# Kernel tuning notes

Measured on AMD Instinct MI355X. Metric: run time of the kernel, lower is better.

The kernel has to match this reference:

```python
import jax, jax.numpy as jnp
import numpy as np

D, H, L, DFF, V = 512, 8, 6, 2048, 32000
PAD = 0

def make_pe(max_len, d):
    pos = jnp.arange(max_len, dtype=jnp.float32)[:, None]
    div = jnp.exp(jnp.arange(0, d, 2, dtype=jnp.float32) * (-np.log(10000.0) / d))
    ang = pos * div  # [max_len, d/2]
    pe = jnp.zeros((max_len, d), jnp.float32)
    pe = pe.at[:, 0::2].set(jnp.sin(ang)).at[:, 1::2].set(jnp.cos(ang))
    return pe

def layernorm(x, g, b, eps=1e-5):
    m = x.mean(-1, keepdims=True)
    v = ((x - m) ** 2).mean(-1, keepdims=True)
    return (x - m) * jax.lax.rsqrt(v + eps) * g + b

def mha(q_in, k_in, v_in, W, Bv, mask):
    # W: [4, D, D] (q,k,v,out); Bv: [4, D]; mask broadcastable to [B,H,Tq,Tk] bool
    b, sq, d = q_in.shape
    hd = d // H
    def proj(x, w, bb):
        y = x @ w + bb
        return y.reshape(x.shape[0], x.shape[1], H, hd).transpose(0, 2, 1, 3)  # bhsd
    Q, K, Vh = proj(q_in, W[0], Bv[0]), proj(k_in, W[1], Bv[1]), proj(v_in, W[2], Bv[2])
    scores = jnp.einsum('bhqd,bhkd->bhqk', Q, K) / np.sqrt(hd).astype(np.float32)
    scores = jnp.where(mask, scores, jnp.float32(-1e9))
    attn = jax.nn.softmax(scores, axis=-1)
    ctx = jnp.einsum('bhqk,bhkd->bhqd', attn, Vh).transpose(0, 2, 1, 3).reshape(b, sq, d)
    return ctx @ W[3] + Bv[3]

def ffn(x, w1, b1, w2, b2):
    return jax.nn.relu(x @ w1 + b1) @ w2 + b2

def setup_inputs() -> dict:
    key = jax.random.key(0)
    ks = jax.random.split(key, 16)
    s = 0.02
    inp = {
        'src': jax.random.randint(ks[0], (8, 512), 0, V, dtype=jnp.int32),
        'tgt': jax.random.randint(ks[1], (8, 512), 0, V, dtype=jnp.int32),
        'src_emb': (jax.random.normal(ks[2], (V, D)) * s).at[PAD].set(0.0),
        'tgt_emb': (jax.random.normal(ks[3], (V, D)) * s).at[PAD].set(0.0),
        'enc_attn_w': jax.random.normal(ks[4], (L, 4, D, D)) * s,
        'enc_attn_b': jnp.zeros((L, 4, D)),
        'enc_ffn_w1': jax.random.normal(ks[5], (L, D, DFF)) * s,
        'enc_ffn_b1': jnp.zeros((L, DFF)),
        'enc_ffn_w2': jax.random.normal(ks[6], (L, DFF, D)) * s,
        'enc_ffn_b2': jnp.zeros((L, D)),
        'enc_ln_g': jnp.ones((L, 2, D)),
        'enc_ln_b': jnp.zeros((L, 2, D)),
        'dec_self_w': jax.random.normal(ks[7], (L, 4, D, D)) * s,
        'dec_self_b': jnp.zeros((L, 4, D)),
        'dec_cross_w': jax.random.normal(ks[8], (L, 4, D, D)) * s,
        'dec_cross_b': jnp.zeros((L, 4, D)),
        'dec_ffn_w1': jax.random.normal(ks[9], (L, D, DFF)) * s,
        'dec_ffn_b1': jnp.zeros((L, DFF)),
        'dec_ffn_w2': jax.random.normal(ks[10], (L, DFF, D)) * s,
        'dec_ffn_b2': jnp.zeros((L, D)),
        'dec_ln_g': jnp.ones((L, 3, D)),
        'dec_ln_b': jnp.zeros((L, 3, D)),
        'out_w': jax.random.normal(ks[11], (D, V)) * s,
        'out_b': jnp.zeros((V,)),
    }
    return inp

def reference(src, tgt, src_emb, tgt_emb, enc_attn_w, enc_attn_b, enc_ffn_w1, enc_ffn_b1,
              enc_ffn_w2, enc_ffn_b2, enc_ln_g, enc_ln_b, dec_self_w, dec_self_b,
              dec_cross_w, dec_cross_b, dec_ffn_w1, dec_ffn_b1, dec_ffn_w2, dec_ffn_b2,
              dec_ln_g, dec_ln_b, out_w, out_b):
    B_, S = src.shape
    T = tgt.shape[1]
    pe = make_pe(max(S, T), D)
    scale = jnp.float32(np.sqrt(D))

    src_pad = (src != PAD)[:, None, None, :]                    # [B,1,1,S]
    causal = jnp.tril(jnp.ones((T, T), bool))                   # [T,T]
    tgt_mask = (tgt != PAD)[:, None, None, :] & causal[None, None]  # [B,1,T,T]

    # encoder (dropout = identity at inference)
    x = src_emb[src] * scale + pe[None, :S]
    for i in range(L):
        a = mha(x, x, x, enc_attn_w[i], enc_attn_b[i], src_pad)
        x = layernorm(x + a, enc_ln_g[i, 0], enc_ln_b[i, 0])
        f = ffn(x, enc_ffn_w1[i], enc_ffn_b1[i], enc_ffn_w2[i], enc_ffn_b2[i])
        x = layernorm(x + f, enc_ln_g[i, 1], enc_ln_b[i, 1])
    memory = x

    # decoder
    y = tgt_emb[tgt] * scale + pe[None, :T]
    for i in range(L):
        a = mha(y, y, y, dec_self_w[i], dec_self_b[i], tgt_mask)
        y = layernorm(y + a, dec_ln_g[i, 0], dec_ln_b[i, 0])
        c = mha(y, memory, memory, dec_cross_w[i], dec_cross_b[i], src_pad)
        y = layernorm(y + c, dec_ln_g[i, 1], dec_ln_b[i, 1])
        f = ffn(y, dec_ffn_w1[i], dec_ffn_b1[i], dec_ffn_w2[i], dec_ffn_b2[i])
        y = layernorm(y + f, dec_ln_g[i, 2], dec_ln_b[i, 2])

    return y @ out_w + out_b  # [B, T, tgt_vocab]
```

## Files before the change

### kernel.cpp

```cpp
#include <hip/hip_runtime.h>
#include <hip/hip_bf16.h>


#define Dm 512
#define Hh 8
#define HD 64
#define Ll 6
#define DFFv 2048
#define Vv 32000
#define Bb 8
#define Ss 512
#define NTOK (Bb * Ss)

typedef __bf16 bf16x8 __attribute__((ext_vector_type(8)));
typedef __bf16 bf16x4 __attribute__((ext_vector_type(4)));
typedef float  f32x4  __attribute__((ext_vector_type(4)));

#define GLOAD16(gp, lp) __builtin_amdgcn_global_load_lds( \
    (const __attribute__((address_space(1))) unsigned int*)(const void*)(gp), \
    (__attribute__((address_space(3))) unsigned int*)(void*)(lp), 16, 0, 0)

__global__ void embed_pe_k(const int* __restrict__ tok, const float* __restrict__ emb,
                           float* __restrict__ out, __bf16* __restrict__ outb, int Slen)
{
    int row = blockIdx.x;
    int s = row % Slen;
    int t = tok[row];
    const float* e = emb + (size_t)t * Dm;
    float* o = out + (size_t)row * Dm;
    __bf16* ob = outb + (size_t)row * Dm;
    for (int dd = threadIdx.x; dd < Dm; dd += blockDim.x) {
        int j = dd >> 1;
        float div = expf((float)(2 * j) * (-9.210340371976184f / 512.0f));
        float ang = (float)s * div;
        float pe = (dd & 1) ? cosf(ang) : sinf(ang);
        float v = e[dd] * 22.627416997969522f + pe;
        o[dd] = v;
        ob[dd] = (__bf16)v;
    }
}

__global__ __launch_bounds__(256) void wtr_k(const float* __restrict__ W,
                                             __bf16* __restrict__ Wt, int K, int N)
{
    __shared__ float t[32][33];
    size_t msz = (size_t)K * N;
    const float* Wm = W + (size_t)blockIdx.z * msz;
    __bf16* Wtm = Wt + (size_t)blockIdx.z * msz;
    int n0 = blockIdx.x * 32, k0 = blockIdx.y * 32;
    int r = threadIdx.x >> 3, c4 = (threadIdx.x & 7) * 4;
    float4 v = *reinterpret_cast<const float4*>(&Wm[(size_t)(k0 + r) * N + n0 + c4]);
    t[r][c4] = v.x; t[r][c4 + 1] = v.y; t[r][c4 + 2] = v.z; t[r][c4 + 3] = v.w;
    __syncthreads();
    int n = threadIdx.x >> 3, kq = (threadIdx.x & 7) * 4;
    bf16x4 o;
    o[0] = (__bf16)t[kq + 0][n]; o[1] = (__bf16)t[kq + 1][n];
    o[2] = (__bf16)t[kq + 2][n]; o[3] = (__bf16)t[kq + 3][n];
    *reinterpret_cast<bf16x4*>(&Wtm[(size_t)(n0 + n) * K + k0 + kq]) = o;
}

template<int BM, int BN, int RELU, int MODE, int SWAPG>
__global__ __launch_bounds__(256) void gemm_mfma_k(const __bf16* __restrict__ A,
                                                   const __bf16* __restrict__ Wt,
                                                   const float* __restrict__ bias,
                                                   void* __restrict__ Cout,
                                                   __bf16* __restrict__ out_k,
                                                   __bf16* __restrict__ out_vT,
                                                   int M, int N, int K)
{
    constexpr int NF_M = BM / 32;
    constexpr int NF_N = BN / 32;
    __shared__ __bf16 As[2][BM * 32];
    __shared__ __bf16 Bs[2][BN * 32];
    const int tid = threadIdx.x;
    const int wave = tid >> 6, lane = tid & 63;
    const int wr = wave >> 1, wc = wave & 1;
    const int row0 = (SWAPG ? blockIdx.x : blockIdx.y) * BM;
    const int col0 = (SWAPG ? blockIdx.y : blockIdx.x) * BN;

    f32x4 acc[NF_M][NF_N] = {};

    const int rsub = lane >> 2;
    const int kel  = (lane & 3) * 8;
    const int fr   = lane & 15;
    const int kg   = lane >> 4;

    auto stage = [&](int buf, int k0) {
        #pragma unroll
        for (int cc = 0; cc < BM / 64; ++cc) {
            int c = wave * (BM / 64) + cc;
            GLOAD16(A + (size_t)(row0 + c * 16 + rsub) * K + k0 + kel,
                    &As[buf][c * 512 + lane * 8]);
        }
        #pragma unroll
        for (int cc = 0; cc < BN / 64; ++cc) {
            int c = wave * (BN / 64) + cc;
            GLOAD16(Wt + (size_t)(col0 + c * 16 + rsub) * K + k0 + kel,
                    &Bs[buf][c * 512 + lane * 8]);
        }
    };

    stage(0, 0);
    __syncthreads();

    const int nk = K >> 5;
    for (int kb = 0; kb < nk; ++kb) {
        int cur = kb & 1;
        if (kb + 1 < nk) stage(cur ^ 1, (kb + 1) * 32);

        const bf16x8* Av = reinterpret_cast<const bf16x8*>(As[cur]);
        const bf16x8* Bv = reinterpret_cast<const bf16x8*>(Bs[cur]);
        bf16x8 af[NF_M], bq[NF_N];
        #pragma unroll
        for (int m = 0; m < NF_M; ++m)
            af[m] = Av[(wr * (BM / 2) + m * 16 + fr) * 4 + kg];
        #pragma unroll
        for (int n = 0; n < NF_N; ++n)
            bq[n] = Bv[(wc * (BN / 2) + n * 16 + fr) * 4 + kg];
        #pragma unroll
        for (int m = 0; m < NF_M; ++m)
            #pragma unroll
            for (int n = 0; n < NF_N; ++n)
                acc[m][n] = __builtin_amdgcn_mfma_f32_16x16x32_bf16(
                    af[m], bq[n], acc[m][n], 0, 0, 0);
        __syncthreads();
    }

    #pragma unroll
    for (int m = 0; m < NF_M; ++m) {
        #pragma unroll
        for (int n = 0; n < NF_N; ++n) {
            int colg = col0 + wc * (BN / 2) + n * 16 + fr;
            float bv = bias[colg];
            #pragma unroll
            for (int j = 0; j < 4; ++j) {
                int row = row0 + wr * (BM / 2) + m * 16 + kg * 4 + j;
                float v = acc[m][n][j] + bv;
                if (RELU) v = fmaxf(v, 0.f);
                if constexpr (MODE == 0) {
                    ((float*)Cout)[(size_t)row * N + colg] = v;
                } else if constexpr (MODE == 1) {
                    ((__bf16*)Cout)[(size_t)row * N + colg] = (__bf16)v;
                } else {
                    int seg = colg >> 9;
                    int c = colg & 511;
                    bool isV = (MODE == 2) ? (seg == 2) : (seg == 1);
                    if (!isV) {
                        __bf16* o = (MODE == 2 && seg == 1) ? out_k : (__bf16*)Cout;
                        o[(size_t)row * 512 + c] = (__bf16)v;
                    } else {
                        int bi = row >> 9, s = row & 511;
                        int hh = c >> 6, f = c & 63;
                        out_vT[(size_t)((bi * 8 + hh) * 64 + f) * 512 + s] = (__bf16)v;
                    }
                }
            }
        }
    }
}

__global__ __launch_bounds__(256) void attn_mfma_k(const __bf16* __restrict__ Qb,
                                                   const __bf16* __restrict__ Kb,
                                                   const __bf16* __restrict__ VbT,
                                                   __bf16* __restrict__ Ob,
                                                   const int* __restrict__ key_tok,
                                                   int causal)
{
    __shared__ __bf16 Ks[2][128 * 64];
    __shared__ __bf16 Vs[2][64 * 128];
    __shared__ __bf16 Pl[4][16 * 128];

    const int tid = threadIdx.x;
    const int w = tid >> 6, lane = tid & 63;
    const int fr = lane & 15, kg = lane >> 4;
    const int q0 = blockIdx.x * 64;
    const int h = blockIdx.y, b = blockIdx.z;
    const int qrow = q0 + w * 16 + fr;
    const int swz = (fr & 7) << 4;

    bf16x8 qf[2];
    {
        const __bf16* qp = Qb + ((size_t)(b * 512 + qrow) * 512 + h * 64 + kg * 8);
        qf[0] = *reinterpret_cast<const bf16x8*>(qp);
        qf[1] = *reinterpret_cast<const bf16x8*>(qp + 32);
    }

    f32x4 po[4] = {};
    float m_run = -3.0e38f, l_run = 0.f;
    __bf16* pw = Pl[w];

    auto stage = [&](int buf, int kk0) {
        #pragma unroll
        for (int c = 0; c < 4; ++c) {
            int ch = c * 256 + tid;
            int r = ch >> 3, gsk = (ch & 7) ^ (r & 7);
            GLOAD16(Kb + ((size_t)(b * 512 + kk0 + r) * 512 + h * 64 + gsk * 8),
                    &Ks[buf][ch * 8]);
            int f = ch >> 4, gsv = (ch & 15) ^ (f & 7);
            GLOAD16(VbT + ((size_t)((b * 8 + h) * 64 + f) * 512 + kk0 + gsv * 8),
                    &Vs[buf][ch * 8]);
        }
    };

    const int kkend = causal ? ((q0 + 64 + 127) & ~127) : 512;
    stage(0, 0);
    __syncthreads();

    for (int kk0 = 0; kk0 < kkend; kk0 += 128) {
        int cur = (kk0 >> 7) & 1;
        if (kk0 + 128 < kkend) stage(cur ^ 1, kk0 + 128);

        unsigned long long vm0 = __ballot(key_tok[b * 512 + kk0 + lane] != 0);
        unsigned long long vm1 = __ballot(key_tok[b * 512 + kk0 + 64 + lane] != 0);

        f32x4 st[8];
        #pragma unroll
        for (int kt = 0; kt < 8; ++kt) {
            f32x4 s = {};
            #pragma unroll
            for (int ks = 0; ks < 2; ++ks) {
                int byte = ((kt * 16 + fr) * 128 + ks * 64 + kg * 16) ^ swz;
                bf16x8 kf = *reinterpret_cast<const bf16x8*>((const char*)Ks[cur] + byte);
                s = __builtin_amdgcn_mfma_f32_16x16x32_bf16(kf, qf[ks], s, 0, 0, 0);
            }
            st[kt] = s;
        }

        float sv[8][4];
        float mloc = -3.0e38f;
        #pragma unroll
        for (int kt = 0; kt < 8; ++kt) {
            unsigned long long vm = (kt < 4) ? vm0 : vm1;
            #pragma unroll
            for (int j = 0; j < 4; ++j) {
                int kl = kt * 16 + kg * 4 + j;
                float s = st[kt][j] * 0.125f;
                bool ok = (vm >> (kl & 63)) & 1ull;
                if (causal && (kk0 + kl > qrow)) ok = false;
                s = ok ? s : -1e9f;
                sv[kt][j] = s;
                mloc = fmaxf(mloc, s);
            }
        }
        mloc = fmaxf(mloc, __shfl_xor(mloc, 16));
        mloc = fmaxf(mloc, __shfl_xor(mloc, 32));
        float m_new = fmaxf(m_run, mloc);
        float scale = __expf(m_run - m_new);
        float ls = 0.f;
        #pragma unroll
        for (int kt = 0; kt < 8; ++kt)
            #pragma unroll
            for (int j = 0; j < 4; ++j) {
                float p = __expf(sv[kt][j] - m_new);
                sv[kt][j] = p;
                ls += p;
            }
        ls += __shfl_xor(ls, 16);
        ls += __shfl_xor(ls, 32);
        l_run = l_run * scale + ls;
        m_run = m_new;

        #pragma unroll
        for (int kt = 0; kt < 8; ++kt)
            #pragma unroll
            for (int c = 0; c < 2; ++c) {
                union { __bf16 hh[2]; unsigned u; } pk;
                pk.hh[0] = (__bf16)sv[kt][2 * c];
                pk.hh[1] = (__bf16)sv[kt][2 * c + 1];
                int byte = (fr * 256 + kt * 32 + kg * 8 + c * 4) ^ swz;
                *reinterpret_cast<unsigned*>((char*)pw + byte) = pk.u;
            }

        {
            int qb4 = kg * 4;
            float s0 = __shfl(scale, qb4 + 0), s1 = __shfl(scale, qb4 + 1);
            float s2 = __shfl(scale, qb4 + 2), s3 = __shfl(scale, qb4 + 3);
            #pragma unroll
            for (int nf = 0; nf < 4; ++nf) {
                po[nf][0] *= s0; po[nf][1] *= s1;
                po[nf][2] *= s2; po[nf][3] *= s3;
            }
        }

        #pragma unroll
        for (int ks2 = 0; ks2 < 4; ++ks2) {
            int pbyte = (fr * 256 + ks2 * 64 + kg * 16) ^ swz;
            bf16x8 pa = *reinterpret_cast<const bf16x8*>((const char*)pw + pbyte);
            #pragma unroll
            for (int nf = 0; nf < 4; ++nf) {
                int vbyte = ((nf * 16 + fr) * 256 + ks2 * 64 + kg * 16) ^ swz;
                bf16x8 vf = *reinterpret_cast<const bf16x8*>((const char*)Vs[cur] + vbyte);
                po[nf] = __builtin_amdgcn_mfma_f32_16x16x32_bf16(pa, vf, po[nf], 0, 0, 0);
            }
        }
        __syncthreads();
    }

    {
        int qb4 = kg * 4;
        float r0 = 1.0f / __shfl(l_run, qb4 + 0);
        float r1 = 1.0f / __shfl(l_run, qb4 + 1);
        float r2 = 1.0f / __shfl(l_run, qb4 + 2);
        float r3 = 1.0f / __shfl(l_run, qb4 + 3);
        #pragma unroll
        for (int nf = 0; nf < 4; ++nf) {
            size_t base = (size_t)(b * 512 + q0 + w * 16 + qb4) * 512 + h * 64 + nf * 16 + fr;
            Ob[base]           = (__bf16)(po[nf][0] * r0);
            Ob[base + 512]     = (__bf16)(po[nf][1] * r1);
            Ob[base + 1024]    = (__bf16)(po[nf][2] * r2);
            Ob[base + 1536]    = (__bf16)(po[nf][3] * r3);
        }
    }
}

__global__ __launch_bounds__(256) void add_ln_k(float* __restrict__ x,
                                                const float* __restrict__ a,
                                                const float* __restrict__ g,
                                                const float* __restrict__ bb,
                                                __bf16* __restrict__ xb)
{
    int row = blockIdx.x;
    size_t base = (size_t)row * Dm;
    int tid = threadIdx.x;
    float v0 = x[base + tid]       + a[base + tid];
    float v1 = x[base + tid + 256] + a[base + tid + 256];
    float s  = v0 + v1;
    float s2 = v0 * v0 + v1 * v1;
    #pragma unroll
    for (int o = 1; o < 64; o <<= 1) {
        s  += __shfl_xor(s, o);
        s2 += __shfl_xor(s2, o);
    }
    __shared__ float red[8];
    int wid = tid >> 6, lane = tid & 63;
    if (lane == 0) { red[wid] = s; red[wid + 4] = s2; }
    __syncthreads();
    s  = red[0] + red[1] + red[2] + red[3];
    s2 = red[4] + red[5] + red[6] + red[7];
    float mean = s * (1.0f / 512.0f);
    float var  = s2 * (1.0f / 512.0f) - mean * mean;
    float rstd = rsqrtf(var + 1e-5f);
    float y0 = (v0 - mean) * rstd * g[tid]       + bb[tid];
    float y1 = (v1 - mean) * rstd * g[tid + 256] + bb[tid + 256];
    x[base + tid]        = y0;
    x[base + tid + 256]  = y1;
    xb[base + tid]       = (__bf16)y0;
    xb[base + tid + 256] = (__bf16)y1;
}

extern "C" void kernel_launch(void* const* d_in, const int* in_sizes, int n_in,
                              void* d_out, int out_size, void* d_ws, size_t ws_size,
                              hipStream_t stream)
{
    const int*   src        = (const int*)  d_in[0];
    const int*   tgt        = (const int*)  d_in[1];
    const float* src_emb    = (const float*)d_in[2];
    const float* tgt_emb    = (const float*)d_in[3];
    const float* enc_attn_w = (const float*)d_in[4];
    const float* enc_attn_b = (const float*)d_in[5];
    const float* enc_ffn_w1 = (const float*)d_in[6];
    const float* enc_ffn_b1 = (const float*)d_in[7];
    const float* enc_ffn_w2 = (const float*)d_in[8];
    const float* enc_ffn_b2 = (const float*)d_in[9];
    const float* enc_ln_g   = (const float*)d_in[10];
    const float* enc_ln_b   = (const float*)d_in[11];
    const float* dec_self_w = (const float*)d_in[12];
    const float* dec_self_b = (const float*)d_in[13];
    const float* dec_cross_w= (const float*)d_in[14];
    const float* dec_cross_b= (const float*)d_in[15];
    const float* dec_ffn_w1 = (const float*)d_in[16];
    const float* dec_ffn_b1 = (const float*)d_in[17];
    const float* dec_ffn_w2 = (const float*)d_in[18];
    const float* dec_ffn_b2 = (const float*)d_in[19];
    const float* dec_ln_g   = (const float*)d_in[20];
    const float* dec_ln_b   = (const float*)d_in[21];
    const float* out_w      = (const float*)d_in[22];
    const float* out_b      = (const float*)d_in[23];

    const size_t NROW = (size_t)NTOK * Dm;
    const size_t NH1  = (size_t)NTOK * DFFv;

    float* ws  = (float*)d_ws;
    float* xe  = ws;
    float* xd  = xe + NROW;
    float* t0  = xd + NROW;

    __bf16* xeb  = (__bf16*)(t0 + NROW);
    __bf16* xdb  = xeb + NROW;
    __bf16* qbb  = xdb + NROW;
    __bf16* kbb  = qbb + NROW;
    __bf16* vbT  = kbb + NROW;
    __bf16* ctxb = vbT + NROW;
    __bf16* h1b  = ctxb + NROW;

    const size_t WSZ  = (size_t)Dm * Dm;
    const size_t FSZ  = (size_t)Dm * DFFv;
    __bf16* w_enc_attn = h1b + NH1;
    __bf16* w_enc_f1   = w_enc_attn + 24 * WSZ;
    __bf16* w_enc_f2   = w_enc_f1 + 6 * FSZ;
    __bf16* w_dec_self = w_enc_f2 + 6 * FSZ;
    __bf16* w_dec_cross= w_dec_self + 24 * WSZ;
    __bf16* w_dec_f1   = w_dec_cross + 24 * WSZ;
    __bf16* w_dec_f2   = w_dec_f1 + 6 * FSZ;
    __bf16* w_out      = w_dec_f2 + 6 * FSZ;

    wtr_k<<<dim3(Dm / 32, Dm / 32, 24), 256, 0, stream>>>(enc_attn_w, w_enc_attn, Dm, Dm);
    wtr_k<<<dim3(DFFv / 32, Dm / 32, 6), 256, 0, stream>>>(enc_ffn_w1, w_enc_f1, Dm, DFFv);
    wtr_k<<<dim3(Dm / 32, DFFv / 32, 6), 256, 0, stream>>>(enc_ffn_w2, w_enc_f2, DFFv, Dm);
    wtr_k<<<dim3(Dm / 32, Dm / 32, 24), 256, 0, stream>>>(dec_self_w, w_dec_self, Dm, Dm);
    wtr_k<<<dim3(Dm / 32, Dm / 32, 24), 256, 0, stream>>>(dec_cross_w, w_dec_cross, Dm, Dm);
    wtr_k<<<dim3(DFFv / 32, Dm / 32, 6), 256, 0, stream>>>(dec_ffn_w1, w_dec_f1, Dm, DFFv);
    wtr_k<<<dim3(Dm / 32, DFFv / 32, 6), 256, 0, stream>>>(dec_ffn_w2, w_dec_f2, DFFv, Dm);
    wtr_k<<<dim3(Vv / 32, Dm / 32, 1), 256, 0, stream>>>(out_w, w_out, Dm, Vv);

    auto gqkv = [&](const __bf16* A, const __bf16* Wt, const float* bias) {
        gemm_mfma_k<64, 128, 0, 2, 0><<<dim3(1536 / 128, NTOK / 64), 256, 0, stream>>>(
            A, Wt, bias, qbb, kbb, vbT, NTOK, 1536, Dm);
    };
    auto gkv = [&](const __bf16* A, const __bf16* Wt, const float* bias) {
        gemm_mfma_k<64, 128, 0, 3, 0><<<dim3(1024 / 128, NTOK / 64), 256, 0, stream>>>(
            A, Wt, bias, kbb, nullptr, vbT, NTOK, 1024, Dm);
    };
    auto g64f = [&](const __bf16* A, const __bf16* Wt, const float* bias, float* C, int K) {
        gemm_mfma_k<64, 64, 0, 0, 0><<<dim3(Dm / 64, NTOK / 64), 256, 0, stream>>>(
            A, Wt, bias, C, nullptr, nullptr, NTOK, Dm, K);
    };
    auto g64b = [&](const __bf16* A, const __bf16* Wt, const float* bias, __bf16* C, int K) {
        gemm_mfma_k<64, 64, 0, 1, 0><<<dim3(Dm / 64, NTOK / 64), 256, 0, stream>>>(
            A, Wt, bias, C, nullptr, nullptr, NTOK, Dm, K);
    };
    auto attn = [&](const __bf16* Q, const __bf16* K, const __bf16* Vt, __bf16* O,
                    const int* kt, int causal) {
        attn_mfma_k<<<dim3(Ss / 64, Hh, Bb), 256, 0, stream>>>(Q, K, Vt, O, kt, causal);
    };
    auto lnorm = [&](float* x, const float* a, const float* g, const float* b, __bf16* xb) {
        add_ln_k<<<NTOK, 256, 0, stream>>>(x, a, g, b, xb);
    };

    embed_pe_k<<<NTOK, 256, 0, stream>>>(src, src_emb, xe, xeb, Ss);
    embed_pe_k<<<NTOK, 256, 0, stream>>>(tgt, tgt_emb, xd, xdb, Ss);

    for (int i = 0; i < Ll; ++i) {
        const __bf16* W = w_enc_attn + (size_t)i * 4 * WSZ;
        const float* Bv = enc_attn_b + (size_t)i * 4 * Dm;
        gqkv(xeb, W, Bv);
        attn(qbb, kbb, vbT, ctxb, src, 0);
        g64f(ctxb, W + 3 * WSZ, Bv + 3 * Dm, t0, Dm);
        lnorm(xe, t0, enc_ln_g + i * 2 * Dm, enc_ln_b + i * 2 * Dm, xeb);
        gemm_mfma_k<128, 128, 1, 1, 0><<<dim3(DFFv / 128, NTOK / 128), 256, 0, stream>>>(
            xeb, w_enc_f1 + (size_t)i * FSZ, enc_ffn_b1 + i * DFFv, h1b, nullptr, nullptr,
            NTOK, DFFv, Dm);
        g64f(h1b, w_enc_f2 + (size_t)i * FSZ, enc_ffn_b2 + i * Dm, t0, DFFv);
        lnorm(xe, t0, enc_ln_g + i * 2 * Dm + Dm, enc_ln_b + i * 2 * Dm + Dm, xeb);
    }

    for (int i = 0; i < Ll; ++i) {
        const __bf16* Wsf = w_dec_self + (size_t)i * 4 * WSZ;
        const float* Bsf = dec_self_b + (size_t)i * 4 * Dm;
        gqkv(xdb, Wsf, Bsf);
        attn(qbb, kbb, vbT, ctxb, tgt, 1);
        g64f(ctxb, Wsf + 3 * WSZ, Bsf + 3 * Dm, t0, Dm);
        lnorm(xd, t0, dec_ln_g + i * 3 * Dm, dec_ln_b + i * 3 * Dm, xdb);

        const __bf16* Wc = w_dec_cross + (size_t)i * 4 * WSZ;
        const float* Bc = dec_cross_b + (size_t)i * 4 * Dm;
        g64b(xdb, Wc + 0 * WSZ, Bc + 0 * Dm, qbb, Dm);
        gkv(xeb, Wc + 1 * WSZ, Bc + 1 * Dm);
        attn(qbb, kbb, vbT, ctxb, src, 0);
        g64f(ctxb, Wc + 3 * WSZ, Bc + 3 * Dm, t0, Dm);
        lnorm(xd, t0, dec_ln_g + i * 3 * Dm + Dm, dec_ln_b + i * 3 * Dm + Dm, xdb);

        gemm_mfma_k<128, 128, 1, 1, 0><<<dim3(DFFv / 128, NTOK / 128), 256, 0, stream>>>(
            xdb, w_dec_f1 + (size_t)i * FSZ, dec_ffn_b1 + i * DFFv, h1b, nullptr, nullptr,
            NTOK, DFFv, Dm);
        g64f(h1b, w_dec_f2 + (size_t)i * FSZ, dec_ffn_b2 + i * Dm, t0, DFFv);
        lnorm(xd, t0, dec_ln_g + i * 3 * Dm + 2 * Dm, dec_ln_b + i * 3 * Dm + 2 * Dm, xdb);
    }

    gemm_mfma_k<128, 256, 0, 0, 1><<<dim3(NTOK / 128, Vv / 256), 256, 0, stream>>>(
        xdb, w_out, out_b, d_out, nullptr, nullptr, NTOK, Vv, Dm);
}
```

Measured before the change: 2.341 ms.

## Use K=64 XOR-swizzled LDS tiles and a 256x256 output-projection GEMM

The generic MFMA GEMM now stages K=64 per iteration, which halves the number of barrier rounds. It stores rows in LDS with an XOR swizzle on the 16-byte chunk index to avoid bank conflicts on fragment reads. A new 512-thread 256x256-tile kernel handles the final vocabulary projection to raise data reuse per block. The cost is more LDS per block: 64 KB double-buffered for the big kernel, which could reduce occupancy. Separately, the SWAPG template flag and the g64b helper are removed.

After: 2.130 ms. 9.0% less time.

```diff
diff --git a/kernel.cpp b/kernel.cpp
--- a/kernel.cpp
+++ b/kernel.cpp
@@ -59,7 +59,7 @@
     *reinterpret_cast<bf16x4*>(&Wtm[(size_t)(n0 + n) * K + k0 + kq]) = o;
 }
 
-template<int BM, int BN, int RELU, int MODE, int SWAPG>
+template<int BM, int BN, int RELU, int MODE>
 __global__ __launch_bounds__(256) void gemm_mfma_k(const __bf16* __restrict__ A,
                                                    const __bf16* __restrict__ Wt,
                                                    const float* __restrict__ bias,
@@ -70,59 +70,65 @@
 {
     constexpr int NF_M = BM / 32;
     constexpr int NF_N = BN / 32;
-    __shared__ __bf16 As[2][BM * 32];
-    __shared__ __bf16 Bs[2][BN * 32];
+    __shared__ __bf16 As[2][BM * 64];
+    __shared__ __bf16 Bs[2][BN * 64];
     const int tid = threadIdx.x;
     const int wave = tid >> 6, lane = tid & 63;
     const int wr = wave >> 1, wc = wave & 1;
-    const int row0 = (SWAPG ? blockIdx.x : blockIdx.y) * BM;
-    const int col0 = (SWAPG ? blockIdx.y : blockIdx.x) * BN;
+    const int row0 = blockIdx.y * BM, col0 = blockIdx.x * BN;
 
     f32x4 acc[NF_M][NF_N] = {};
 
-    const int rsub = lane >> 2;
-    const int kel  = (lane & 3) * 8;
-    const int fr   = lane & 15;
-    const int kg   = lane >> 4;
+    const int fr = lane & 15;
+    const int kg = lane >> 4;
 
     auto stage = [&](int buf, int k0) {
         #pragma unroll
-        for (int cc = 0; cc < BM / 64; ++cc) {
-            int c = wave * (BM / 64) + cc;
-            GLOAD16(A + (size_t)(row0 + c * 16 + rsub) * K + k0 + kel,
-                    &As[buf][c * 512 + lane * 8]);
-        }
-        #pragma unroll
-        for (int cc = 0; cc < BN / 64; ++cc) {
-            int c = wave * (BN / 64) + cc;
-            GLOAD16(Wt + (size_t)(col0 + c * 16 + rsub) * K + k0 + kel,
-                    &Bs[buf][c * 512 + lane * 8]);
+        for (int cc = 0; cc < BM / 32; ++cc) {
+            int g = cc * 256 + tid;
+            int r = g >> 3, cs = g & 7, gs = cs ^ (r & 7);
+            GLOAD16(A + (size_t)(row0 + r) * K + k0 + gs * 8, &As[buf][g * 8]);
+        }
+        #pragma unroll
+        for (int cc = 0; cc < BN / 32; ++cc) {
+            int g = cc * 256 + tid;
+            int r = g >> 3, cs = g & 7, gs = cs ^ (r & 7);
+            GLOAD16(Wt + (size_t)(col0 + r) * K + k0 + gs * 8, &Bs[buf][g * 8]);
         }
     };
 
     stage(0, 0);
     __syncthreads();
 
-    const int nk = K >> 5;
+    const int nk = K >> 6;
     for (int kb = 0; kb < nk; ++kb) {
         int cur = kb & 1;
-        if (kb + 1 < nk) stage(cur ^ 1, (kb + 1) * 32);
-
-        const bf16x8* Av = reinterpret_cast<const bf16x8*>(As[cur]);
-        const bf16x8* Bv = reinterpret_cast<const bf16x8*>(Bs[cur]);
-        bf16x8 af[NF_M], bq[NF_N];
-        #pragma unroll
-        for (int m = 0; m < NF_M; ++m)
-            af[m] = Av[(wr * (BM / 2) + m * 16 + fr) * 4 + kg];
-        #pragma unroll
-        for (int n = 0; n < NF_N; ++n)
-            bq[n] = Bv[(wc * (BN / 2) + n * 16 + fr) * 4 + kg];
-        #pragma unroll
-        for (int m = 0; m < NF_M; ++m)
-            #pragma unroll
-            for (int n = 0; n < NF_N; ++n)
-                acc[m][n] = __builtin_amdgcn_mfma_f32_16x16x32_bf16(
-                    af[m], bq[n], acc[m][n], 0, 0, 0);
+        if (kb + 1 < nk) stage(cur ^ 1, (kb + 1) * 64);
+
+        const char* Ab = (const char*)As[cur];
+        const char* Bbp = (const char*)Bs[cur];
+        #pragma unroll
+        for (int ks = 0; ks < 2; ++ks) {
+            bf16x8 af[NF_M], bq[NF_N];
+            #pragma unroll
+            for (int m = 0; m < NF_M; ++m) {
+                int ar = wr * (BM / 2) + m * 16 + fr;
+                af[m] = *reinterpret_cast<const bf16x8*>(
+                    Ab + ar * 128 + (((ks * 4 + kg) ^ (ar & 7)) << 4));
+            }
+            #pragma unroll
+            for (int n = 0; n < NF_N; ++n) {
+                int br = wc * (BN / 2) + n * 16 + fr;
+                bq[n] = *reinterpret_cast<const bf16x8*>(
+                    Bbp + br * 128 + (((ks * 4 + kg) ^ (br & 7)) << 4));
+            }
+            #pragma unroll
+            for (int m = 0; m < NF_M; ++m)
+                #pragma unroll
+                for (int n = 0; n < NF_N; ++n)
+                    acc[m][n] = __builtin_amdgcn_mfma_f32_16x16x32_bf16(
+                        af[m], bq[n], acc[m][n], 0, 0, 0);
+        }
         __syncthreads();
     }
 
@@ -154,6 +160,89 @@
                         out_vT[(size_t)((bi * 8 + hh) * 64 + f) * 512 + s] = (__bf16)v;
                     }
                 }
+            }
+        }
+    }
+}
+
+__global__ __launch_bounds__(512) void gemm256_k(const __bf16* __restrict__ A,
+                                                 const __bf16* __restrict__ Wt,
+                                                 const float* __restrict__ bias,
+                                                 float* __restrict__ C,
+                                                 int M, int N, int K)
+{
+    __shared__ __bf16 As[2][256 * 64];
+    __shared__ __bf16 Bs[2][256 * 64];
+    const int tid = threadIdx.x;
+    const int wave = tid >> 6, lane = tid & 63;
+    const int wr = wave >> 2, wc = wave & 3;
+    const int row0 = blockIdx.x * 256, col0 = blockIdx.y * 256;
+
+    f32x4 acc[8][4] = {};
+
+    const int fr = lane & 15;
+    const int kg = lane >> 4;
+
+    auto stage = [&](int buf, int k0) {
+        #pragma unroll
+        for (int cc = 0; cc < 4; ++cc) {
+            int g = cc * 512 + tid;
+            int r = g >> 3, cs = g & 7, gs = cs ^ (r & 7);
+            GLOAD16(A + (size_t)(row0 + r) * K + k0 + gs * 8, &As[buf][g * 8]);
+        }
+        #pragma unroll
+        for (int cc = 0; cc < 4; ++cc) {
+            int g = cc * 512 + tid;
+            int r = g >> 3, cs = g & 7, gs = cs ^ (r & 7);
+            GLOAD16(Wt + (size_t)(col0 + r) * K + k0 + gs * 8, &Bs[buf][g * 8]);
+        }
+    };
+
+    stage(0, 0);
+    __syncthreads();
+
+    const int nk = K >> 6;
+    for (int kb = 0; kb < nk; ++kb) {
+        int cur = kb & 1;
+        if (kb + 1 < nk) stage(cur ^ 1, (kb + 1) * 64);
+
+        const char* Ab = (const char*)As[cur];
+        const char* Bbp = (const char*)Bs[cur];
+        #pragma unroll
+        for (int ks = 0; ks < 2; ++ks) {
+            bf16x8 af[8], bq[4];
+            #pragma unroll
+            for (int m = 0; m < 8; ++m) {
+                int ar = wr * 128 + m * 16 + fr;
+                af[m] = *reinterpret_cast<const bf16x8*>(
+                    Ab + ar * 128 + (((ks * 4 + kg) ^ (ar & 7)) << 4));
+            }
+            #pragma unroll
+            for (int n = 0; n < 4; ++n) {
+                int br = wc * 64 + n * 16 + fr;
+                bq[n] = *reinterpret_cast<const bf16x8*>(
+                    Bbp + br * 128 + (((ks * 4 + kg) ^ (br & 7)) << 4));
+            }
+            #pragma unroll
+            for (int m = 0; m < 8; ++m)
+                #pragma unroll
+                for (int n = 0; n < 4; ++n)
+                    acc[m][n] = __builtin_amdgcn_mfma_f32_16x16x32_bf16(
+                        af[m], bq[n], acc[m][n], 0, 0, 0);
+        }
+        __syncthreads();
+    }
+
+    #pragma unroll
+    for (int m = 0; m < 8; ++m) {
+        #pragma unroll
+        for (int n = 0; n < 4; ++n) {
+            int colg = col0 + wc * 64 + n * 16 + fr;
+            float bv = bias[colg];
+            #pragma unroll
+            for (int j = 0; j < 4; ++j) {
+                int row = row0 + wr * 128 + m * 16 + kg * 4 + j;
+                C[(size_t)row * N + colg] = acc[m][n][j] + bv;
             }
         }
     }
@@ -414,19 +503,15 @@
     wtr_k<<<dim3(Vv / 32, Dm / 32, 1), 256, 0, stream>>>(out_w, w_out, Dm, Vv);
 
     auto gqkv = [&](const __bf16* A, const __bf16* Wt, const float* bias) {
-        gemm_mfma_k<64, 128, 0, 2, 0><<<dim3(1536 / 128, NTOK / 64), 256, 0, stream>>>(
+        gemm_mfma_k<64, 128, 0, 2><<<dim3(1536 / 128, NTOK / 64), 256, 0, stream>>>(
             A, Wt, bias, qbb, kbb, vbT, NTOK, 1536, Dm);
     };
     auto gkv = [&](const __bf16* A, const __bf16* Wt, const float* bias) {
-        gemm_mfma_k<64, 128, 0, 3, 0><<<dim3(1024 / 128, NTOK / 64), 256, 0, stream>>>(
+        gemm_mfma_k<64, 128, 0, 3><<<dim3(1024 / 128, NTOK / 64), 256, 0, stream>>>(
             A, Wt, bias, kbb, nullptr, vbT, NTOK, 1024, Dm);
     };
     auto g64f = [&](const __bf16* A, const __bf16* Wt, const float* bias, float* C, int K) {
-        gemm_mfma_k<64, 64, 0, 0, 0><<<dim3(Dm / 64, NTOK / 64), 256, 0, stream>>>(
-            A, Wt, bias, C, nullptr, nullptr, NTOK, Dm, K);
-    };
-    auto g64b = [&](const __bf16* A, const __bf16* Wt, const float* bias, __bf16* C, int K) {
-        gemm_mfma_k<64, 64, 0, 1, 0><<<dim3(Dm / 64, NTOK / 64), 256, 0, stream>>>(
+        gemm_mfma_k<64, 64, 0, 0><<<dim3(Dm / 64, NTOK / 64), 256, 0, stream>>>(
             A, Wt, bias, C, nullptr, nullptr, NTOK, Dm, K);
     };
     auto attn = [&](const __bf16* Q, const __bf16* K, const __bf16* Vt, __bf16* O,
@@ -447,7 +532,7 @@
         attn(qbb, kbb, vbT, ctxb, src, 0);
         g64f(ctxb, W + 3 * WSZ, Bv + 3 * Dm, t0, Dm);
         lnorm(xe, t0, enc_ln_g + i * 2 * Dm, enc_ln_b + i * 2 * Dm, xeb);
-        gemm_mfma_k<128, 128, 1, 1, 0><<<dim3(DFFv / 128, NTOK / 128), 256, 0, stream>>>(
+        gemm_mfma_k<128, 128, 1, 1><<<dim3(DFFv / 128, NTOK / 128), 256, 0, stream>>>(
             xeb, w_enc_f1 + (size_t)i * FSZ, enc_ffn_b1 + i * DFFv, h1b, nullptr, nullptr,
             NTOK, DFFv, Dm);
         g64f(h1b, w_enc_f2 + (size_t)i * FSZ, enc_ffn_b2 + i * Dm, t0, DFFv);
@@ -464,19 +549,20 @@
 
         const __bf16* Wc = w_dec_cross + (size_t)i * 4 * WSZ;
         const float* Bc = dec_cross_b + (size_t)i * 4 * Dm;
-        g64b(xdb, Wc + 0 * WSZ, Bc + 0 * Dm, qbb, Dm);
+        gemm_mfma_k<64, 64, 0, 1><<<dim3(Dm / 64, NTOK / 64), 256, 0, stream>>>(
+            xdb, Wc + 0 * WSZ, Bc + 0 * Dm, qbb, nullptr, nullptr, NTOK, Dm, Dm);
         gkv(xeb, Wc + 1 * WSZ, Bc + 1 * Dm);
         attn(qbb, kbb, vbT, ctxb, src, 0);
         g64f(ctxb, Wc + 3 * WSZ, Bc + 3 * Dm, t0, Dm);
         lnorm(xd, t0, dec_ln_g + i * 3 * Dm + Dm, dec_ln_b + i * 3 * Dm + Dm, xdb);
 
-        gemm_mfma_k<128, 128, 1, 1, 0><<<dim3(DFFv / 128, NTOK / 128), 256, 0, stream>>>(
+        gemm_mfma_k<128, 128, 1, 1><<<dim3(DFFv / 128, NTOK / 128), 256, 0, stream>>>(
             xdb, w_dec_f1 + (size_t)i * FSZ, dec_ffn_b1 + i * DFFv, h1b, nullptr, nullptr,
             NTOK, DFFv, Dm);
         g64f(h1b, w_dec_f2 + (size_t)i * FSZ, dec_ffn_b2 + i * Dm, t0, DFFv);
         lnorm(xd, t0, dec_ln_g + i * 3 * Dm + 2 * Dm, dec_ln_b + i * 3 * Dm + 2 * Dm, xdb);
     }
 
-    gemm_mfma_k<128, 256, 0, 0, 1><<<dim3(NTOK / 128, Vv / 256), 256, 0, stream>>>(
-        xdb, w_out, out_b, d_out, nullptr, nullptr, NTOK, Vv, Dm);
-}
+    gemm256_k<<<dim3(NTOK / 256, Vv / 256), 512, 0, stream>>>(
+        xdb, w_out, out_b, (float*)d_out, NTOK, Vv, Dm);
+}
```
